# Kernel optimization log

Measured on AMD Instinct MI355X. Metric: run time of the kernel, lower is better.

Reference implementation:

```python
import jax, jax.numpy as jnp
import numpy as np

N_HEAD = 16
T0 = 1.0        # eta schedule reference time
C_LOG = 3.0     # fixed eta(t) = C_LOG * log(t / T0)  (mode='log', non-learnable default)
ETA_CLIP = 50.0 # eta clamped to [-ETA_CLIP, ETA_CLIP] before exponentiation


def setup_inputs() -> dict:
    key = jax.random.key(0)
    k0, k1, k2 = jax.random.split(key, 3)
    B, T, D = 2, 2048, 1024
    x = jax.random.normal(k0, (B, T, D), dtype=jnp.float32)
    ln_weight = jnp.ones((D,), dtype=jnp.float32)  # LayerNorm weight (bias=False per cfg)
    c_attn_w = jax.random.normal(k1, (3 * D, D), dtype=jnp.float32) * 0.02  # torch Linear weight [3D, D]
    c_proj_w = jax.random.normal(k2, (D, D), dtype=jnp.float32) * 0.02      # output proj [D, D]
    # theta_h = inv_softplus(1.0) so that step size h = softplus(theta_h) = 1.0
    theta_h = jnp.asarray(np.log(np.expm1(1.0)), dtype=jnp.float32)
    return {"x": x, "ln_weight": ln_weight, "c_attn_w": c_attn_w,
            "c_proj_w": c_proj_w, "theta_h": theta_h}


def _layer_norm(x, w, eps=1e-5):
    mu = jnp.mean(x, axis=-1, keepdims=True)
    var = jnp.var(x, axis=-1, keepdims=True)
    return (x - mu) * jax.lax.rsqrt(var + eps) * w


def reference(x, ln_weight, c_attn_w, c_proj_w, theta_h):
    B, T, D = x.shape
    H = N_HEAD
    hd = D // H

    y = _layer_norm(x, ln_weight)
    qkv = jnp.einsum('btd,ed->bte', y, c_attn_w)        # [B, T, 3D]
    q, k, v = jnp.split(qkv, 3, axis=-1)
    q = q.reshape(B, T, H, hd).transpose(0, 2, 1, 3)    # [B, H, T, hd]
    k = k.reshape(B, T, H, hd).transpose(0, 2, 1, 3)
    v = v.reshape(B, T, H, hd).transpose(0, 2, 1, 3)

    # time-dependent conformal/symplectic scaling: t_i = t0 + h*i, eta = c_log*log(t/t0)
    h = jax.nn.softplus(theta_h)
    t = T0 + h * jnp.arange(T, dtype=jnp.float32)
    eta = jnp.clip(C_LOG * jnp.log(t / T0), -ETA_CLIP, ETA_CLIP)  # [T]
    q = q * jnp.exp(eta)[None, None, :, None]    # query scaled by exp(+eta(t_i))
    k = k * jnp.exp(-eta)[None, None, :, None]   # key scaled by exp(-eta(t_j))

    att = jnp.einsum('bhqd,bhkd->bhqk', q, k) / jnp.sqrt(jnp.float32(hd))
    mask = jnp.tril(jnp.ones((T, T), dtype=bool))  # causal: keep j <= i
    att = jnp.where(mask[None, None], att, -jnp.inf)
    att = jax.nn.softmax(att, axis=-1)

    out = jnp.einsum('bhqk,bhkd->bhqd', att, v)
    out = out.transpose(0, 2, 1, 3).reshape(B, T, D)
    return jnp.einsum('btd,ed->bte', out, c_proj_w)
```

## Files before the change

kernel.cpp:

```cpp
#include <hip/hip_runtime.h>
#include <stdint.h>
#include <stddef.h>

typedef __attribute__((ext_vector_type(8))) short short8;
typedef __attribute__((ext_vector_type(4))) float float4v;

#define T_SEQ 2048
#define D_MODEL 1024
#define NH 16
#define HD 64

static __device__ __forceinline__ unsigned short f2bf(float f) {
  unsigned u = __builtin_bit_cast(unsigned, f);
  u += 0x7fffu + ((u >> 16) & 1u);
  return (unsigned short)(u >> 16);
}
static __device__ __forceinline__ float bf2f(unsigned short h) {
  unsigned u = ((unsigned)h) << 16;
  return __builtin_bit_cast(float, u);
}
static __device__ __forceinline__ float4v mfma16(short8 a, short8 b, float4v c) {
  return __builtin_amdgcn_mfma_f32_16x16x32_bf16(a, b, c, 0, 0, 0);
}
static __device__ __forceinline__ void split3(float f, unsigned short& h0,
                                              unsigned short& h1, unsigned short& h2) {
  h0 = f2bf(f);
  float r1 = f - bf2f(h0);
  h1 = f2bf(r1);
  float r2 = r1 - bf2f(h1);
  h2 = f2bf(r2);
}
static __device__ __forceinline__ void split2(float f, unsigned short& h0, unsigned short& h1) {
  h0 = f2bf(f);
  h1 = f2bf(f - bf2f(h0));
}

static __device__ __forceinline__ void stage16(const unsigned short* g, unsigned short* l) {
#if __has_builtin(__builtin_amdgcn_global_load_lds)
  __builtin_amdgcn_global_load_lds(
      (const __attribute__((address_space(1))) unsigned int*)g,
      (__attribute__((address_space(3))) unsigned int*)l, 16, 0, 0);
#else
  *(short8*)l = *(const short8*)g;
#endif
}

__global__ __launch_bounds__(256) void prep_kernel(
    const float* x, const float* wgt, const float* attn_w, const float* theta,
    unsigned short* y0, unsigned short* y1, unsigned short* y2,
    unsigned short* W0, unsigned short* W1, unsigned short* W2,
    float* E, float* Einv) {
  __shared__ float rs[4], rq[4];
  int bx = blockIdx.x;
  int tid = threadIdx.x;
  if (bx < 4096) {
    int row = bx;
    const float* xr = x + (size_t)row * D_MODEL;
    float v[4];
    float sum = 0.f, ssq = 0.f;
    for (int it = 0; it < 4; ++it) {
      float f = xr[tid + 256 * it];
      v[it] = f;
      sum += f; ssq += f * f;
    }
    for (int off = 32; off >= 1; off >>= 1) {
      sum += __shfl_xor(sum, off, 64);
      ssq += __shfl_xor(ssq, off, 64);
    }
    int w = tid >> 6;
    if ((tid & 63) == 0) { rs[w] = sum; rq[w] = ssq; }
    __syncthreads();
    sum = rs[0] + rs[1] + rs[2] + rs[3];
    ssq = rq[0] + rq[1] + rq[2] + rq[3];
    float mu = sum * (1.0f / D_MODEL);
    float var = ssq * (1.0f / D_MODEL) - mu * mu;
    float rstd = rsqrtf(var + 1e-5f);
    for (int it = 0; it < 4; ++it) {
      int d = tid + 256 * it;
      float y = (v[it] - mu) * rstd * wgt[d];
      unsigned short h0, h1, h2;
      split3(y, h0, h1, h2);
      size_t o = (size_t)row * D_MODEL + d;
      y0[o] = h0; y1[o] = h1; y2[o] = h2;
    }
  } else if (bx < 5632) {
    size_t base = ((size_t)(bx - 4096) * 256 + tid) * 8;
    int row = (int)(base >> 10);
    short8 a, b, c;
    for (int j = 0; j < 8; ++j) {
      unsigned short h0, h1, h2;
      split3(attn_w[base + j], h0, h1, h2);
      a[j] = (short)h0; b[j] = (short)h1; c[j] = (short)h2;
    }
    *(short8*)(W0 + base) = a;
    *(short8*)(W1 + base) = b;
    if (row < 2048) *(short8*)(W2 + base) = c;
  } else {
    int i = (bx - 5632) * 256 + tid;
    if (i < T_SEQ) {
      float th = theta[0];
      float h = log1pf(expf(th));
      float t = 1.0f + h * (float)i;
      float eta = 3.0f * logf(t);
      eta = fminf(fmaxf(eta, -50.0f), 50.0f);
      E[i] = expf(eta);
      Einv[i] = expf(-eta);
    }
  }
}

__global__ __launch_bounds__(256) void conv_pw(const float* src, unsigned short* P0,
                                               unsigned short* P1) {
  size_t base = ((size_t)blockIdx.x * 256 + threadIdx.x) * 8;
  short8 a, b;
  for (int j = 0; j < 8; ++j) {
    unsigned short h0, h1;
    split2(src[base + j], h0, h1);
    a[j] = (short)h0; b[j] = (short)h1;
  }
  *(short8*)(P0 + base) = a;
  *(short8*)(P1 + base) = b;
}


#define RD_A(SL, MF)                                                            \
  (*(const short8*)(lds_u + (SL) * 12288 + ((wm * 64 + (MF) * 16 + ln) * 32) +  \
                    ((q4 ^ (ln & 3)) * 8)))
#define RD_B(SL, NF)                                                            \
  (*(const short8*)(lds_u + (SL) * 12288 + 8192 +                               \
                    ((wn * 64 + (NF) * 16 + ln) * 32) + ((q4 ^ (ln & 3)) * 8)))

#define STG_A(SL, AP, KI)                                                       \
  do {                                                                          \
    const unsigned short* g0 =                                                  \
        (AP) + (size_t)(m0 + srow4) * 1024 + (KI) + scol4;                      \
    stage16(g0, lds_u + (SL) * 12288 + tid * 8);                                \
    stage16(g0 + 128 * 1024, lds_u + (SL) * 12288 + 4096 + tid * 8);            \
  } while (0)

#define STG_B(SL, BP, KI)                                                       \
  do {                                                                          \
    const unsigned short* g0 =                                                  \
        (BP) + (size_t)(brow0 + srow4) * 1024 + (KI) + scol4;                   \
    stage16(g0, lds_u + (SL) * 12288 + 8192 + tid * 8);                         \
  } while (0)

#define ASEL(tb) ((tb) == 5 ? y2 : (((tb) & 1) ? y1 : y0))
#define BSEL(tb) (isV ? ((tb) < 2 ? W0 : W1)                                    \
                      : ((tb) < 2 ? W0 : ((tb) < 4 ? W1 : ((tb) == 4 ? W2 : W0))))

#define SBAR __builtin_amdgcn_s_barrier()
#define SCHED0 __builtin_amdgcn_sched_barrier(0)

#define PHASE(SLOT)                                                             \
  {                                                                             \
    short8 a0 = RD_A(SLOT, 0), a1 = RD_A(SLOT, 1);                              \
    short8 a2 = RD_A(SLOT, 2), a3 = RD_A(SLOT, 3);                              \
    short8 b0 = RD_B(SLOT, 0), b1 = RD_B(SLOT, 1);                              \
    short8 b2 = RD_B(SLOT, 2), b3 = RD_B(SLOT, 3);                              \
    bool pref = (t + 3 < NKT);                                                  \
    if (pref) {                                                                 \
      int tt = t + 3, tb = tt >> 5, ki = (tt & 31) << 5;                        \
      const unsigned short* Ap = ASEL(tb);                                      \
      const unsigned short* Bp = BSEL(tb);                                      \
      STG_A((SLOT + 3) & 3, Ap, ki);                                            \
      STG_B((SLOT + 3) & 3, Bp, ki);                                            \
    }                                                                           \
    SCHED0; SBAR;                                                               \
    asm volatile("s_waitcnt lgkmcnt(0)" ::: "memory");                          \
    SCHED0;                                                                     \
    __builtin_amdgcn_s_setprio(1);                                              \
    acc[0][0] = mfma16(a0, b0, acc[0][0]);                                      \
    acc[0][1] = mfma16(a0, b1, acc[0][1]);                                      \
    acc[0][2] = mfma16(a0, b2, acc[0][2]);                                      \
    acc[0][3] = mfma16(a0, b3, acc[0][3]);                                      \
    acc[1][0] = mfma16(a1, b0, acc[1][0]);                                      \
    acc[1][1] = mfma16(a1, b1, acc[1][1]);                                      \
    acc[1][2] = mfma16(a1, b2, acc[1][2]);                                      \
    acc[1][3] = mfma16(a1, b3, acc[1][3]);                                      \
    acc[2][0] = mfma16(a2, b0, acc[2][0]);                                      \
    acc[2][1] = mfma16(a2, b1, acc[2][1]);                                      \
    acc[2][2] = mfma16(a2, b2, acc[2][2]);                                      \
    acc[2][3] = mfma16(a2, b3, acc[2][3]);                                      \
    acc[3][0] = mfma16(a3, b0, acc[3][0]);                                      \
    acc[3][1] = mfma16(a3, b1, acc[3][1]);                                      \
    acc[3][2] = mfma16(a3, b2, acc[3][2]);                                      \
    acc[3][3] = mfma16(a3, b3, acc[3][3]);                                      \
    __builtin_amdgcn_s_setprio(0);                                              \
    SCHED0;                                                                     \
    if (pref) { asm volatile("s_waitcnt vmcnt(6)" ::: "memory"); }              \
    else      { asm volatile("s_waitcnt vmcnt(0)" ::: "memory"); }              \
    SBAR;                                                                       \
    ++t;                                                                        \
  }

__global__ __launch_bounds__(512, 2) void qkv8(
    const unsigned short* __restrict__ y0, const unsigned short* __restrict__ y1,
    const unsigned short* __restrict__ y2, const unsigned short* __restrict__ W0,
    const unsigned short* __restrict__ W1, const unsigned short* __restrict__ W2,
    const float* __restrict__ E, const float* __restrict__ Einv,
    float* __restrict__ Qf, unsigned short* __restrict__ K0,
    unsigned short* __restrict__ K1, unsigned short* __restrict__ K2,
    unsigned short* __restrict__ VbT) {
  extern __shared__ unsigned short lds_u[];
  int tid = threadIdx.x;
  int w = tid >> 6, lane = tid & 63, q4 = lane >> 4, ln = lane & 15;
  int wm = w >> 1, wn = w & 1;

  int bid = blockIdx.x, bx, by;
  if (bid < 256) {
    int wg = ((bid & 7) << 5) | (bid >> 3);
    by = wg >> 4; bx = wg & 15;
  } else {
    int vid = bid - 256;
    int wg = ((vid & 7) << 4) | (vid >> 3);
    by = wg >> 3; bx = 16 + (wg & 7);
  }
  int m0 = by * 256;
  bool isV = (bx >= 16);
  int NKT = isV ? 96 : 192;
  int brow0 = isV ? (2048 + (bx - 16) * 128) : bx * 128;

  int srow4 = tid >> 2;
  int scol4 = ((tid & 3) ^ (srow4 & 3)) * 8;

  float4v zero = {0.f, 0.f, 0.f, 0.f};
  float4v acc[4][4];
#pragma unroll
  for (int mf = 0; mf < 4; ++mf)
#pragma unroll
    for (int nf = 0; nf < 4; ++nf) acc[mf][nf] = zero;

  {
    const unsigned short* Ap = ASEL(0);
    const unsigned short* Bp = BSEL(0);
    STG_A(0, Ap, 0);  STG_B(0, Ap == Ap ? Bp : Bp, 0);
    STG_A(1, Ap, 32); STG_B(1, Bp, 32);
    STG_A(2, Ap, 64); STG_B(2, Bp, 64);
  }
  asm volatile("s_waitcnt vmcnt(6)" ::: "memory");
  SBAR;

  int t = 0;
  int nit = NKT >> 2;
  for (int it = 0; it < nit; ++it) {
    PHASE(0)
    PHASE(1)
    PHASE(2)
    PHASE(3)
  }

  int bi = m0 >> 11, m0g = m0 & 2047;
  if (bx < 8) {
    float* Ql = (float*)lds_u;
    for (int g = 0; g < 2; ++g) {
      if (wn == g) {
#pragma unroll
        for (int mf = 0; mf < 4; ++mf)
#pragma unroll
          for (int nf = 0; nf < 4; ++nf)
#pragma unroll
            for (int r = 0; r < 4; ++r) {
              int rl = wm * 64 + mf * 16 + q4 * 4 + r;
              int tg = m0g + rl;
              Ql[rl * 64 + nf * 16 + ln] = acc[mf][nf][r] * (E[tg] * 0.1803368801f);
            }
      }
      __syncthreads();
      int h = bx * 2 + g;
      float* dst = Qf + ((size_t)(bi * NH + h) * T_SEQ + m0g) * HD;
      for (int itc = 0; itc < 8; ++itc) {
        int idx = itc * 512 + tid;
        *(float4v*)(dst + idx * 4) = *(const float4v*)(Ql + idx * 4);
      }
      __syncthreads();
    }
  } else if (bx < 16) {
    unsigned short* Kl = lds_u;
    for (int g = 0; g < 2; ++g) {
      if (wn == g) {
#pragma unroll
        for (int mf = 0; mf < 4; ++mf)
#pragma unroll
          for (int nf = 0; nf < 4; ++nf)
#pragma unroll
            for (int r = 0; r < 4; ++r) {
              int rl = wm * 64 + mf * 16 + q4 * 4 + r;
              int tg = m0g + rl;
              unsigned short h0, h1, h2;
              split3(acc[mf][nf][r] * Einv[tg], h0, h1, h2);
              int o = rl * 64 + nf * 16 + ln;
              Kl[o] = h0; Kl[16384 + o] = h1; Kl[32768 + o] = h2;
            }
      }
      __syncthreads();
      int h = (bx - 8) * 2 + g;
      size_t base = ((size_t)(bi * NH + h) * T_SEQ + m0g) * HD;
      for (int itc = 0; itc < 4; ++itc) {
        int idx = itc * 512 + tid;
        *(short8*)(K0 + base + idx * 8) = *(const short8*)(Kl + idx * 8);
        *(short8*)(K1 + base + idx * 8) = *(const short8*)(Kl + 16384 + idx * 8);
        *(short8*)(K2 + base + idx * 8) = *(const short8*)(Kl + 32768 + idx * 8);
      }
      __syncthreads();
    }
  } else {
    unsigned short* Vl = lds_u;
    for (int g = 0; g < 2; ++g) {
      if (wn == g) {
#pragma unroll
        for (int mf = 0; mf < 4; ++mf)
#pragma unroll
          for (int nf = 0; nf < 4; ++nf)
#pragma unroll
            for (int r = 0; r < 4; ++r) {
              int rl = wm * 64 + mf * 16 + q4 * 4 + r;
              int d = nf * 16 + ln;
              Vl[d * 256 + rl] = f2bf(acc[mf][nf][r]);
            }
      }
      __syncthreads();
      int h = (bx - 16) * 2 + g;
      unsigned short* dst = VbT + (size_t)(bi * NH + h) * HD * T_SEQ + m0g;
      for (int itc = 0; itc < 4; ++itc) {
        int idx = itc * 512 + tid;
        int d = idx >> 5, c = idx & 31;
        *(short8*)(dst + (size_t)d * T_SEQ + c * 8) = *(const short8*)(Vl + d * 256 + c * 8);
      }
      __syncthreads();
    }
  }
}
#undef RD_A
#undef RD_B
#undef STG_A
#undef STG_B
#undef ASEL
#undef BSEL
#undef PHASE
#undef SBAR
#undef SCHED0

#define ATTN_STAGE(BUF, J0)                                                   \
  for (int i_ = 0; i_ < 2; ++i_) {                                            \
    size_t go_ = (size_t)((J0) + srow + i_ * 32) * 64 + scd * 8;              \
    int lo_ = tid * 8 + i_ * 2048;                                            \
    stage16(Kb0 + go_, &Ks[BUF][0][lo_]);                                     \
    stage16(Kb1 + go_, &Ks[BUF][1][lo_]);                                     \
    stage16(Kb2 + go_, &Ks[BUF][2][lo_]);                                     \
    stage16(Vb + (size_t)(srow + i_ * 32) * T_SEQ + (J0) + scd * 8,           \
            &Vs[BUF][lo_]);                                                   \
  }

#define ATTN_STEP(JT, DIAG)                                                   \
  {                                                                           \
    const int cur_ = (JT) & 1;                                                \
    float p[4][4];                                                            \
    for (int c = 0; c < 4; ++c) {                                             \
      float4v s = zero;                                                       \
      for (int ks = 0; ks < 2; ++ks) {                                        \
        int koff = ((c * 16 + ln) * 8 + ((ks * 4 + q4) ^ swz)) * 8;           \
        short8 k0v = *(const short8*)&Ks[cur_][0][koff];                      \
        short8 k1v = *(const short8*)&Ks[cur_][1][koff];                      \
        short8 k2v = *(const short8*)&Ks[cur_][2][koff];                      \
        s = mfma16(qa[ks][0], k0v, s);                                        \
        s = mfma16(qa[ks][1], k0v, s);                                        \
        s = mfma16(qa[ks][0], k1v, s);                                        \
        s = mfma16(qa[ks][1], k1v, s);                                        \
        s = mfma16(qa[ks][0], k2v, s);                                        \
        s = mfma16(qa[ks][2], k0v, s);                                        \
      }                                                                       \
      if (DIAG) {                                                             \
        int jrow = (JT) * 64 + c * 16 + ln;                                   \
        for (int r = 0; r < 4; ++r)                                           \
          if (jrow > ibase + q4 * 4 + r) s[r] = -3e38f;                       \
      }                                                                       \
      for (int r = 0; r < 4; ++r) p[c][r] = s[r];                             \
    }                                                                         \
    float alpha[4], mnew[4];                                                  \
    for (int r = 0; r < 4; ++r) {                                             \
      float tm = fmaxf(fmaxf(p[0][r], p[1][r]), fmaxf(p[2][r], p[3][r]));     \
      for (int off = 8; off >= 1; off >>= 1)                                  \
        tm = fmaxf(tm, __shfl_xor(tm, off, 16));                              \
      mnew[r] = fmaxf(m_r[r], tm);                                            \
      alpha[r] = exp2f(m_r[r] - mnew[r]);                                     \
      m_r[r] = mnew[r];                                                       \
    }                                                                         \
    for (int c = 0; c < 4; ++c)                                               \
      for (int r = 0; r < 4; ++r) p[c][r] = exp2f(p[c][r] - mnew[r]);         \
    for (int c = 0; c < 4; ++c)                                               \
      for (int r = 0; r < 4; ++r) oacc[c][r] *= alpha[r];                     \
    for (int r = 0; r < 4; ++r) lacc[r] *= alpha[r];                          \
    __asm__ __volatile__("" ::: "memory");                                    \
    for (int c = 0; c < 4; ++c)                                               \
      for (int r = 0; r < 4; ++r)                                             \
        Plds[w][q4 * 4 + r][c * 16 + ln] =                                    \
            (unsigned short)(__builtin_bit_cast(unsigned, p[c][r]) >> 16);    \
    __asm__ __volatile__("" ::: "memory");                                    \
    for (int ks = 0; ks < 2; ++ks) {                                          \
      short8 pa = *(const short8*)&Plds[w][ln][ks * 32 + q4 * 8];             \
      for (int c = 0; c < 4; ++c) {                                           \
        int voff = ((c * 16 + ln) * 8 + ((ks * 4 + q4) ^ swz)) * 8;           \
        short8 vb = *(const short8*)&Vs[cur_][voff];                          \
        oacc[c] = mfma16(pa, vb, oacc[c]);                                    \
      }                                                                       \
      lacc = mfma16(pa, ones, lacc);                                          \
    }                                                                         \
    __asm__ __volatile__("" ::: "memory");                                    \
  }

__global__ __launch_bounds__(256) void attn_kernel(
    const float* Qf, const unsigned short* K0, const unsigned short* K1,
    const unsigned short* K2, const unsigned short* VbT,
    unsigned short* Ob0, unsigned short* Ob1) {
  __shared__ unsigned short Ks[2][3][4096];
  __shared__ unsigned short Vs[2][4096];
  __shared__ unsigned short Plds[4][16][72];
  int tid = threadIdx.x;
  int w = tid >> 6, lane = tid & 63, q4 = lane >> 4, ln = lane & 15;
  int bidx = blockIdx.x;
  int bh = ((bidx & 7) << 2) | ((bidx >> 3) & 3);
  int px = bidx >> 5;
  const float* Qb = Qf + (size_t)bh * T_SEQ * HD;
  const unsigned short* Kb0 = K0 + (size_t)bh * T_SEQ * HD;
  const unsigned short* Kb1 = K1 + (size_t)bh * T_SEQ * HD;
  const unsigned short* Kb2 = K2 + (size_t)bh * T_SEQ * HD;
  const unsigned short* Vb = VbT + (size_t)bh * HD * T_SEQ;
  int b = bh >> 4, hh = bh & 15;
  float4v zero = {0.f, 0.f, 0.f, 0.f};
  short8 ones;
  for (int j = 0; j < 8; ++j) ones[j] = (short)(unsigned short)0x3F80;

  int srow = tid >> 3, scs = tid & 7;
  int scd = scs ^ (srow & 7);
  int swz = ln & 7;

  for (int half = 0; half < 2; ++half) {
    int qt = half ? (31 - px) : px;
    int q0 = qt * 64;
    int ibase = q0 + w * 16;

    short8 qa[2][3];
    {
      const float* qp = Qb + (size_t)(ibase + ln) * HD;
      for (int ks = 0; ks < 2; ++ks) {
        float f[8];
        *(float4v*)&f[0] = *(const float4v*)(qp + ks * 32 + q4 * 8);
        *(float4v*)&f[4] = *(const float4v*)(qp + ks * 32 + q4 * 8 + 4);
        for (int j = 0; j < 8; ++j) {
          unsigned short h0, h1, h2;
          split3(f[j], h0, h1, h2);
          qa[ks][0][j] = (short)h0; qa[ks][1][j] = (short)h1; qa[ks][2][j] = (short)h2;
        }
      }
    }

    float m_r[4] = {-3e38f, -3e38f, -3e38f, -3e38f};
    float4v lacc = zero;
    float4v oacc[4];
    for (int c = 0; c < 4; ++c) oacc[c] = zero;

    __syncthreads();
    ATTN_STAGE(0, 0)
    for (int jt = 0; jt < qt; ++jt) {
      __syncthreads();
      ATTN_STAGE((jt + 1) & 1, (jt + 1) * 64)
      ATTN_STEP(jt, 0)
    }
    __syncthreads();
    ATTN_STEP(qt, 1)

    for (int c = 0; c < 4; ++c)
      for (int r = 0; r < 4; ++r) {
        int i = ibase + q4 * 4 + r;
        float val = oacc[c][r] / lacc[r];
        unsigned short h0, h1;
        split2(val, h0, h1);
        size_t o = ((size_t)(b * T_SEQ + i)) * D_MODEL + hh * 64 + c * 16 + ln;
        Ob0[o] = h0; Ob1[o] = h1;
      }
  }
}
#undef ATTN_STAGE
#undef ATTN_STEP

__global__ __launch_bounds__(256) void proj_gemm(
    const unsigned short* A0, const unsigned short* A1,
    const unsigned short* P0, const unsigned short* P1, float* out) {
  __shared__ unsigned short SB[4 * 4096];
  int tid = threadIdx.x;
  int w = tid >> 6, lane = tid & 63, q4 = lane >> 4, ln = lane & 15;
  int wr = w >> 1, wc = w & 1;
  int n0g = blockIdx.x * 128;
  int m0 = blockIdx.y * 128;
  const unsigned short* Asrc[2] = {A0, A1};
  const unsigned short* Bsrc[2] = {P0, P1};

  float4v zero = {0.f, 0.f, 0.f, 0.f};
  float4v acc[4][4];
  for (int mt = 0; mt < 4; ++mt)
    for (int ct = 0; ct < 4; ++ct) acc[mt][ct] = zero;

  int srow = tid >> 2, kpart = tid & 3;
  unsigned lds_off = (unsigned)tid * 16;

  for (int k0 = 0; k0 < D_MODEL; k0 += 32) {
    __syncthreads();
    for (int i = 0; i < 2; ++i) {
      size_t arow = (size_t)(m0 + srow + i * 64) * D_MODEL + k0 + kpart * 8;
      size_t brow = (size_t)(n0g + srow + i * 64) * D_MODEL + k0 + kpart * 8;
      for (int s = 0; s < 2; ++s) {
        stage16(Asrc[s] + arow, (unsigned short*)((char*)(SB + s * 4096) + lds_off + i * 4096));
        stage16(Bsrc[s] + brow, (unsigned short*)((char*)(SB + (2 + s) * 4096) + lds_off + i * 4096));
      }
    }
    __syncthreads();

    short8 af[4][2];
    for (int mt = 0; mt < 4; ++mt)
      for (int s = 0; s < 2; ++s)
        af[mt][s] = *(const short8*)(SB + s * 4096 + (wr * 64 + mt * 16 + ln) * 32 + q4 * 8);
    for (int ct = 0; ct < 4; ++ct) {
      int brow = (wc * 64 + ct * 16 + ln) * 32 + q4 * 8;
      short8 b0 = *(const short8*)(SB + 2 * 4096 + brow);
      short8 b1 = *(const short8*)(SB + 3 * 4096 + brow);
      for (int mt = 0; mt < 4; ++mt) {
        float4v a = acc[mt][ct];
        a = mfma16(af[mt][0], b0, a);
        a = mfma16(af[mt][1], b0, a);
        a = mfma16(af[mt][0], b1, a);
        acc[mt][ct] = a;
      }
    }
  }

  for (int mt = 0; mt < 4; ++mt)
    for (int ct = 0; ct < 4; ++ct)
      for (int r = 0; r < 4; ++r) {
        int gm = m0 + wr * 64 + mt * 16 + q4 * 4 + r;
        int col = n0g + wc * 64 + ct * 16 + ln;
        out[(size_t)gm * D_MODEL + col] = acc[mt][ct][r];
      }
}

extern "C" void kernel_launch(void* const* d_in, const int* in_sizes, int n_in,
                              void* d_out, int out_size, void* d_ws, size_t ws_size,
                              hipStream_t stream) {
  const float* x      = (const float*)d_in[0];
  const float* ln_w   = (const float*)d_in[1];
  const float* attn_w = (const float*)d_in[2];
  const float* proj_w = (const float*)d_in[3];
  const float* theta  = (const float*)d_in[4];
  float* out = (float*)d_out;

  char* ws = (char*)d_ws;
  const size_t SZY  = (size_t)4096 * 1024 * 2;
  const size_t SZW  = (size_t)3072 * 1024 * 2;
  const size_t SZW2 = (size_t)2048 * 1024 * 2;
  const size_t SZQ  = (size_t)2 * 16 * 2048 * 64 * 4;
  const size_t SZK  = (size_t)2 * 16 * 2048 * 64 * 2;

  unsigned short* y0 = (unsigned short*)(ws);
  unsigned short* y1 = (unsigned short*)(ws + SZY);
  unsigned short* y2 = (unsigned short*)(ws + 2 * SZY);
  unsigned short* W0 = (unsigned short*)(ws + 3 * SZY);
  unsigned short* W1 = (unsigned short*)(ws + 3 * SZY + SZW);
  unsigned short* W2 = (unsigned short*)(ws + 3 * SZY + 2 * SZW);
  float* Qf          = (float*)(ws + 3 * SZY + 2 * SZW + SZW2);
  unsigned short* K0 = (unsigned short*)(ws + 3 * SZY + 2 * SZW + SZW2 + SZQ);
  unsigned short* K1 = (unsigned short*)(ws + 3 * SZY + 2 * SZW + SZW2 + SZQ + SZK);
  float* E           = (float*)(ws + 3 * SZY + 2 * SZW + SZW2 + SZQ + 2 * SZK);
  float* Einv        = E + T_SEQ;
  unsigned short* Ob0 = y0;
  unsigned short* Ob1 = y1;
  unsigned short* PW0 = y2;
  unsigned short* PW1 = y2 + (size_t)1024 * 1024;
  unsigned short* VbT = (unsigned short*)d_out;
  unsigned short* K2  = (unsigned short*)((char*)d_out + SZK);

  size_t needed = 3 * SZY + 2 * SZW + SZW2 + SZQ + 2 * SZK + 2 * T_SEQ * 4;
  if (ws_size < needed) return;

  static int lds_cfg = 0;
  if (!lds_cfg) {
    hipFuncSetAttribute((const void*)qkv8,
                        hipFuncAttributeMaxDynamicSharedMemorySize, 98304);
    lds_cfg = 1;
  }

  prep_kernel<<<dim3(5640), dim3(256), 0, stream>>>(x, ln_w, attn_w, theta,
                                                    y0, y1, y2, W0, W1, W2, E, Einv);
  qkv8<<<dim3(384), dim3(512), 98304, stream>>>(y0, y1, y2, W0, W1, W2, E, Einv,
                                                Qf, K0, K1, K2, VbT);
  conv_pw<<<dim3(512), dim3(256), 0, stream>>>(proj_w, PW0, PW1);
  attn_kernel<<<dim3(512), dim3(256), 0, stream>>>(Qf, K0, K1, K2, VbT, Ob0, Ob1);
  proj_gemm<<<dim3(8, 32), dim3(256), 0, stream>>>(Ob0, Ob1, PW0, PW1, out);
}
```

Measured before the change: 407.3 us.

## Shrink QKV GEMM ring to three LDS stages and change LDS swizzle

The QKV GEMM's LDS ring buffer drops from four stages to three, with prefetch distance two instead of three. Dynamic LDS falls from 96KB to 72KB and launch bounds now request four waves per SIMD instead of two, aiming for more resident blocks per CU. The K epilogue is split into half-tiles so its staging fits the smaller LDS footprint. The XOR swizzle for LDS tiles changes to use (row>>1)&3 in both the QKV kernel and proj_gemm, to reduce bank conflicts; the shallower prefetch risks exposing more global-load latency.

Measured after the change: 377.7 us (median of 2 runs). 1.08x faster.

```diff
diff --git a/kernel.cpp b/kernel.cpp
--- a/kernel.cpp
+++ b/kernel.cpp
@@ -123,26 +123,20 @@
 }
 
 
-#define RD_A(SL, MF)                                                            \
-  (*(const short8*)(lds_u + (SL) * 12288 + ((wm * 64 + (MF) * 16 + ln) * 32) +  \
-                    ((q4 ^ (ln & 3)) * 8)))
-#define RD_B(SL, NF)                                                            \
-  (*(const short8*)(lds_u + (SL) * 12288 + 8192 +                               \
-                    ((wn * 64 + (NF) * 16 + ln) * 32) + ((q4 ^ (ln & 3)) * 8)))
-
-#define STG_A(SL, AP, KI)                                                       \
+#define RD_A(BUF, MF)                                                           \
+  (*(const short8*)(lds_u + (BUF) * 12288 + (wm * 64 + (MF) * 16 + ln) * 32 +   \
+                    slot8))
+#define RD_B(BUF, NF)                                                           \
+  (*(const short8*)(lds_u + (BUF) * 12288 + 8192 +                              \
+                    (wn * 64 + (NF) * 16 + ln) * 32 + slot8))
+
+#define STG(BUF, AP, BP, KI)                                                    \
   do {                                                                          \
-    const unsigned short* g0 =                                                  \
-        (AP) + (size_t)(m0 + srow4) * 1024 + (KI) + scol4;                      \
-    stage16(g0, lds_u + (SL) * 12288 + tid * 8);                                \
-    stage16(g0 + 128 * 1024, lds_u + (SL) * 12288 + 4096 + tid * 8);            \
-  } while (0)
-
-#define STG_B(SL, BP, KI)                                                       \
-  do {                                                                          \
-    const unsigned short* g0 =                                                  \
-        (BP) + (size_t)(brow0 + srow4) * 1024 + (KI) + scol4;                   \
-    stage16(g0, lds_u + (SL) * 12288 + 8192 + tid * 8);                         \
+    const unsigned short* ga = (AP) + (size_t)(m0 + srow) * 1024 + (KI) + kswz8; \
+    stage16(ga, lds_u + (BUF) * 12288 + tid * 8);                               \
+    stage16(ga + 128 * 1024, lds_u + (BUF) * 12288 + 4096 + tid * 8);           \
+    stage16((BP) + (size_t)(brow0 + srow) * 1024 + (KI) + kswz8,                \
+            lds_u + (BUF) * 12288 + 8192 + tid * 8);                            \
   } while (0)
 
 #define ASEL(tb) ((tb) == 5 ? y2 : (((tb) & 1) ? y1 : y0))
@@ -152,19 +146,18 @@
 #define SBAR __builtin_amdgcn_s_barrier()
 #define SCHED0 __builtin_amdgcn_sched_barrier(0)
 
-#define PHASE(SLOT)                                                             \
+#define PHASE(BUF, PBUF)                                                        \
   {                                                                             \
-    short8 a0 = RD_A(SLOT, 0), a1 = RD_A(SLOT, 1);                              \
-    short8 a2 = RD_A(SLOT, 2), a3 = RD_A(SLOT, 3);                              \
-    short8 b0 = RD_B(SLOT, 0), b1 = RD_B(SLOT, 1);                              \
-    short8 b2 = RD_B(SLOT, 2), b3 = RD_B(SLOT, 3);                              \
-    bool pref = (t + 3 < NKT);                                                  \
+    short8 a0 = RD_A(BUF, 0), a1 = RD_A(BUF, 1);                                \
+    short8 a2 = RD_A(BUF, 2), a3 = RD_A(BUF, 3);                                \
+    short8 b0 = RD_B(BUF, 0), b1 = RD_B(BUF, 1);                                \
+    short8 b2 = RD_B(BUF, 2), b3 = RD_B(BUF, 3);                                \
+    bool pref = (t + 2 < NKT);                                                  \
     if (pref) {                                                                 \
-      int tt = t + 3, tb = tt >> 5, ki = (tt & 31) << 5;                        \
+      int tt = t + 2, tb = tt >> 5, ki = (tt & 31) << 5;                        \
       const unsigned short* Ap = ASEL(tb);                                      \
       const unsigned short* Bp = BSEL(tb);                                      \
-      STG_A((SLOT + 3) & 3, Ap, ki);                                            \
-      STG_B((SLOT + 3) & 3, Bp, ki);                                            \
+      STG(PBUF, Ap, Bp, ki);                                                    \
     }                                                                           \
     SCHED0; SBAR;                                                               \
     asm volatile("s_waitcnt lgkmcnt(0)" ::: "memory");                          \
@@ -188,13 +181,13 @@
     acc[3][3] = mfma16(a3, b3, acc[3][3]);                                      \
     __builtin_amdgcn_s_setprio(0);                                              \
     SCHED0;                                                                     \
-    if (pref) { asm volatile("s_waitcnt vmcnt(6)" ::: "memory"); }              \
+    if (pref) { asm volatile("s_waitcnt vmcnt(3)" ::: "memory"); }              \
     else      { asm volatile("s_waitcnt vmcnt(0)" ::: "memory"); }              \
     SBAR;                                                                       \
     ++t;                                                                        \
   }
 
-__global__ __launch_bounds__(512, 2) void qkv8(
+__global__ __launch_bounds__(512, 4) void qkv_ring(
     const unsigned short* __restrict__ y0, const unsigned short* __restrict__ y1,
     const unsigned short* __restrict__ y2, const unsigned short* __restrict__ W0,
     const unsigned short* __restrict__ W1, const unsigned short* __restrict__ W2,
@@ -206,6 +199,9 @@
   int tid = threadIdx.x;
   int w = tid >> 6, lane = tid & 63, q4 = lane >> 4, ln = lane & 15;
   int wm = w >> 1, wn = w & 1;
+  int slot8 = (q4 ^ ((ln >> 1) & 3)) * 8;
+  int srow = tid >> 2;
+  int kswz8 = ((tid & 3) ^ ((srow >> 1) & 3)) * 8;
 
   int bid = blockIdx.x, bx, by;
   if (bid < 256) {
@@ -221,9 +217,6 @@
   int NKT = isV ? 96 : 192;
   int brow0 = isV ? (2048 + (bx - 16) * 128) : bx * 128;
 
-  int srow4 = tid >> 2;
-  int scol4 = ((tid & 3) ^ (srow4 & 3)) * 8;
-
   float4v zero = {0.f, 0.f, 0.f, 0.f};
   float4v acc[4][4];
 #pragma unroll
@@ -234,20 +227,18 @@
   {
     const unsigned short* Ap = ASEL(0);
     const unsigned short* Bp = BSEL(0);
-    STG_A(0, Ap, 0);  STG_B(0, Ap == Ap ? Bp : Bp, 0);
-    STG_A(1, Ap, 32); STG_B(1, Bp, 32);
-    STG_A(2, Ap, 64); STG_B(2, Bp, 64);
-  }
-  asm volatile("s_waitcnt vmcnt(6)" ::: "memory");
+    STG(0, Ap, Bp, 0);
+    STG(1, Ap, Bp, 32);
+  }
+  asm volatile("s_waitcnt vmcnt(3)" ::: "memory");
   SBAR;
 
   int t = 0;
-  int nit = NKT >> 2;
+  int nit = NKT / 3;
   for (int it = 0; it < nit; ++it) {
-    PHASE(0)
-    PHASE(1)
-    PHASE(2)
-    PHASE(3)
+    PHASE(0, 2)
+    PHASE(1, 0)
+    PHASE(2, 1)
   }
 
   int bi = m0 >> 11, m0g = m0 & 2047;
@@ -277,33 +268,34 @@
     }
   } else if (bx < 16) {
     unsigned short* Kl = lds_u;
-    for (int g = 0; g < 2; ++g) {
-      if (wn == g) {
-#pragma unroll
-        for (int mf = 0; mf < 4; ++mf)
-#pragma unroll
-          for (int nf = 0; nf < 4; ++nf)
-#pragma unroll
-            for (int r = 0; r < 4; ++r) {
-              int rl = wm * 64 + mf * 16 + q4 * 4 + r;
-              int tg = m0g + rl;
-              unsigned short h0, h1, h2;
-              split3(acc[mf][nf][r] * Einv[tg], h0, h1, h2);
-              int o = rl * 64 + nf * 16 + ln;
-              Kl[o] = h0; Kl[16384 + o] = h1; Kl[32768 + o] = h2;
-            }
-      }
-      __syncthreads();
-      int h = (bx - 8) * 2 + g;
-      size_t base = ((size_t)(bi * NH + h) * T_SEQ + m0g) * HD;
-      for (int itc = 0; itc < 4; ++itc) {
-        int idx = itc * 512 + tid;
-        *(short8*)(K0 + base + idx * 8) = *(const short8*)(Kl + idx * 8);
-        *(short8*)(K1 + base + idx * 8) = *(const short8*)(Kl + 16384 + idx * 8);
-        *(short8*)(K2 + base + idx * 8) = *(const short8*)(Kl + 32768 + idx * 8);
-      }
-      __syncthreads();
-    }
+    for (int g = 0; g < 2; ++g)
+      for (int half = 0; half < 2; ++half) {
+        if (wn == g && (wm >> 1) == half) {
+#pragma unroll
+          for (int mf = 0; mf < 4; ++mf)
+#pragma unroll
+            for (int nf = 0; nf < 4; ++nf)
+#pragma unroll
+              for (int r = 0; r < 4; ++r) {
+                int rlh = (wm & 1) * 64 + mf * 16 + q4 * 4 + r;
+                int tg = m0g + half * 128 + rlh;
+                unsigned short h0, h1, h2;
+                split3(acc[mf][nf][r] * Einv[tg], h0, h1, h2);
+                int o = rlh * 64 + nf * 16 + ln;
+                Kl[o] = h0; Kl[8192 + o] = h1; Kl[16384 + o] = h2;
+              }
+        }
+        __syncthreads();
+        int h = (bx - 8) * 2 + g;
+        size_t base = ((size_t)(bi * NH + h) * T_SEQ + m0g + half * 128) * HD;
+        for (int itc = 0; itc < 2; ++itc) {
+          int idx = itc * 512 + tid;
+          *(short8*)(K0 + base + idx * 8) = *(const short8*)(Kl + idx * 8);
+          *(short8*)(K1 + base + idx * 8) = *(const short8*)(Kl + 8192 + idx * 8);
+          *(short8*)(K2 + base + idx * 8) = *(const short8*)(Kl + 16384 + idx * 8);
+        }
+        __syncthreads();
+      }
   } else {
     unsigned short* Vl = lds_u;
     for (int g = 0; g < 2; ++g) {
@@ -333,8 +325,7 @@
 }
 #undef RD_A
 #undef RD_B
-#undef STG_A
-#undef STG_B
+#undef STG
 #undef ASEL
 #undef BSEL
 #undef PHASE
@@ -502,13 +493,15 @@
     for (int ct = 0; ct < 4; ++ct) acc[mt][ct] = zero;
 
   int srow = tid >> 2, kpart = tid & 3;
+  int kswz = kpart ^ ((srow >> 1) & 3);
+  int slot8 = (q4 ^ ((ln >> 1) & 3)) * 8;
   unsigned lds_off = (unsigned)tid * 16;
 
   for (int k0 = 0; k0 < D_MODEL; k0 += 32) {
     __syncthreads();
     for (int i = 0; i < 2; ++i) {
-      size_t arow = (size_t)(m0 + srow + i * 64) * D_MODEL + k0 + kpart * 8;
-      size_t brow = (size_t)(n0g + srow + i * 64) * D_MODEL + k0 + kpart * 8;
+      size_t arow = (size_t)(m0 + srow + i * 64) * D_MODEL + k0 + kswz * 8;
+      size_t brow = (size_t)(n0g + srow + i * 64) * D_MODEL + k0 + kswz * 8;
       for (int s = 0; s < 2; ++s) {
         stage16(Asrc[s] + arow, (unsigned short*)((char*)(SB + s * 4096) + lds_off + i * 4096));
         stage16(Bsrc[s] + brow, (unsigned short*)((char*)(SB + (2 + s) * 4096) + lds_off + i * 4096));
@@ -519,9 +512,9 @@
     short8 af[4][2];
     for (int mt = 0; mt < 4; ++mt)
       for (int s = 0; s < 2; ++s)
-        af[mt][s] = *(const short8*)(SB + s * 4096 + (wr * 64 + mt * 16 + ln) * 32 + q4 * 8);
+        af[mt][s] = *(const short8*)(SB + s * 4096 + (wr * 64 + mt * 16 + ln) * 32 + slot8);
     for (int ct = 0; ct < 4; ++ct) {
-      int brow = (wc * 64 + ct * 16 + ln) * 32 + q4 * 8;
+      int brow = (wc * 64 + ct * 16 + ln) * 32 + slot8;
       short8 b0 = *(const short8*)(SB + 2 * 4096 + brow);
       short8 b1 = *(const short8*)(SB + 3 * 4096 + brow);
       for (int mt = 0; mt < 4; ++mt) {
@@ -583,15 +576,15 @@
 
   static int lds_cfg = 0;
   if (!lds_cfg) {
-    hipFuncSetAttribute((const void*)qkv8,
-                        hipFuncAttributeMaxDynamicSharedMemorySize, 98304);
+    hipFuncSetAttribute((const void*)qkv_ring,
+                        hipFuncAttributeMaxDynamicSharedMemorySize, 73728);
     lds_cfg = 1;
   }
 
   prep_kernel<<<dim3(5640), dim3(256), 0, stream>>>(x, ln_w, attn_w, theta,
                                                     y0, y1, y2, W0, W1, W2, E, Einv);
-  qkv8<<<dim3(384), dim3(512), 98304, stream>>>(y0, y1, y2, W0, W1, W2, E, Einv,
-                                                Qf, K0, K1, K2, VbT);
+  qkv_ring<<<dim3(384), dim3(512), 73728, stream>>>(y0, y1, y2, W0, W1, W2, E, Einv,
+                                                    Qf, K0, K1, K2, VbT);
   conv_pw<<<dim3(512), dim3(256), 0, stream>>>(proj_w, PW0, PW1);
   attn_kernel<<<dim3(512), dim3(256), 0, stream>>>(Qf, K0, K1, K2, VbT, Ob0, Ob1);
   proj_gemm<<<dim3(8, 32), dim3(256), 0, stream>>>(Ob0, Ob1, PW0, PW1, out);
```
